# Performance work log

Hardware: AMD Instinct MI355X
Metric: run time of the kernel (lower is better)

The kernel has to match this reference:

```python
import jax, jax.numpy as jnp
import numpy as np

B, N, D, H = 32, 8192, 128, 128


def setup_inputs() -> dict:
    key = jax.random.key(0)
    ks = jax.random.split(key, 9)
    s = lambda k, shp, fan: jax.random.normal(k, shp, jnp.float32) / np.sqrt(fan)
    return {
        "x": jax.random.normal(ks[0], (B, N, D), jnp.float32),
        "Wg1": s(ks[1], (D, H), D), "bg1": jnp.zeros((H,), jnp.float32),
        "Wg2": s(ks[2], (H, 1), H), "bg2": jnp.zeros((1,), jnp.float32),
        "Wn1": s(ks[3], (D, H), D), "bn1": jnp.zeros((H,), jnp.float32),
        "Wn2": s(ks[4], (H, H), H), "bn2": jnp.zeros((H,), jnp.float32),
    }


def reference(x, Wg1, bg1, Wg2, bg2, Wn1, bn1, Wn2, bn2):
    # gate_nn: Linear -> SiLU -> Linear(->1); scores per node
    gate = jnp.einsum("bnd,dh->bnh", x, Wg1) + bg1
    gate = jax.nn.silu(gate)
    gate = jnp.einsum("bnh,ho->bno", gate, Wg2) + bg2  # [B,N,1]
    # nn: Linear -> SiLU -> Linear; transformed node features
    h = jax.nn.silu(jnp.einsum("bnd,dh->bnh", x, Wn1) + bn1)
    h = jnp.einsum("bnh,hk->bnk", h, Wn2) + bn2  # [B,N,H]
    # segment softmax over nodes of each graph (segments == batch dim here)
    attn = jax.nn.softmax(gate, axis=1)  # [B,N,1]
    # weighted-sum pooling per graph
    return jnp.sum(attn * h, axis=1)  # [B,H]
```

## Files before the change

### kernel.cpp

```cpp
#include <hip/hip_runtime.h>

#define B_ 32
#define N_ 8192
#define D_ 128
#define H_ 128
#define R_ (B_ * N_)

#define NBLK 4096

typedef _Float16 f16;
typedef __attribute__((ext_vector_type(4))) _Float16 f16x4;
typedef __attribute__((ext_vector_type(8))) _Float16 f16x8;
typedef __attribute__((ext_vector_type(4))) float f32x4;

static constexpr size_t WPACK_OFF = 0;
static constexpr size_t VPART_OFF = 98304;
static constexpr size_t SPART_OFF = VPART_OFF + (size_t)NBLK * 128 * 4;

__device__ __forceinline__ float silu_f(float v) {
    return v * __builtin_amdgcn_rcpf(1.0f + __expf(-v));
}

__device__ __forceinline__ f32x4 mfma16(f16x8 a, f16x8 b, f32x4 c) {
    return __builtin_amdgcn_mfma_f32_16x16x32_f16(a, b, c, 0, 0, 0);
}

__global__ void k0_prepack(const float* __restrict__ Wg1,
                           const float* __restrict__ Wn1,
                           const float* __restrict__ Wn2,
                           f16* __restrict__ wp) {
    int tid = blockIdx.x * 256 + threadIdx.x;
    int m    = tid >> 14;
    int r    = tid & 16383;
    int j    = r & 7;
    int lane = (r >> 3) & 63;
    int kc   = (r >> 9) & 3;
    int nt   = r >> 11;
    int k = kc * 32 + (lane >> 4) * 8 + j;
    int n = nt * 16 + (lane & 15);
    const float* W = (m == 0) ? Wg1 : (m == 1) ? Wn1 : Wn2;
    wp[tid] = (f16)W[k * 128 + n];
}

__global__ __launch_bounds__(256, 3) void k1_fused(
        const float* __restrict__ x,
        const float* __restrict__ bg1, const float* __restrict__ wg2,
        const float* __restrict__ bg2, const float* __restrict__ bn1,
        const f16* __restrict__ wp,
        float* __restrict__ vpart, float* __restrict__ spart) {
    __shared__ f16 xlds[64 * 128];
    __shared__ f16 h1lds[64 * 128];
    __shared__ float gpart[4][64];

    const int tid  = threadIdx.x;
    const int w    = tid >> 6;
    const int lane = tid & 63;
    const int q    = lane >> 4;
    const int c    = lane & 15;

    const long rowbase = (long)blockIdx.x * 64;
    const float4* xg = (const float4*)x + rowbase * 32;
    float4 xv[8];
#pragma unroll
    for (int s = 0; s < 8; ++s) xv[s] = xg[s * 256 + tid];

    const f16x8* wpv = (const f16x8*)wp;
    f16x8 fg1[2][4], fn1[2][4];
#pragma unroll
    for (int s = 0; s < 2; ++s)
#pragma unroll
        for (int kc = 0; kc < 4; ++kc) {
            int base = ((2 * w + s) * 4 + kc) * 64 + lane;
            fg1[s][kc] = wpv[base];
            fn1[s][kc] = wpv[2048 + base];
        }
    float bg1q[2][4], wg2q[2][4], bn1q[2][4];
#pragma unroll
    for (int s = 0; s < 2; ++s)
#pragma unroll
        for (int r = 0; r < 4; ++r) {
            int col = (2 * w + s) * 16 + q * 4 + r;
            bg1q[s][r] = bg1[col];
            wg2q[s][r] = wg2[col];
            bn1q[s][r] = bn1[col];
        }
    const float bg2v = bg2[0];

    const int loh_e = (q * 16 + (c ^ q)) * 8;
    const int loh_o = (q * 16 + (c ^ (q | 4))) * 8;
    int h1wb[2];
#pragma unroll
    for (int s = 0; s < 2; ++s) {
        int q2 = s * 2 + (q >> 1);
        int v2 = ((w & 1) << 2) | q2;
        h1wb[s] = w * 512 + (q2 * 16 + (c ^ v2)) * 8 + (q & 1) * 4;
    }

#pragma unroll
    for (int s = 0; s < 8; ++s) {
        int e   = s * 256 + tid;
        int row = e >> 5, c4 = e & 31;
        int mt = row >> 4, cc = row & 15;
        int kc = c4 >> 3, qq = (c4 >> 1) & 3, j = (c4 & 1) * 4;
        int sw = (c4 >> 1) & 7;
        float4 vv = xv[s];
        f16x4 hv = {(f16)vv.x, (f16)vv.y, (f16)vv.z, (f16)vv.w};
        *(f16x4*)&xlds[((mt * 4 + kc) * 64 + qq * 16 + (cc ^ sw)) * 8 + j] = hv;
    }
    __syncthreads();

#pragma unroll
    for (int mt = 0; mt < 4; ++mt) {
        f16x8 a[4];
#pragma unroll
        for (int kc = 0; kc < 4; ++kc)
            a[kc] = *(const f16x8*)&xlds[(mt * 4 + kc) * 512 +
                                         ((kc & 1) ? loh_o : loh_e)];
        f32x4 ag[2] = {{0.f,0.f,0.f,0.f},{0.f,0.f,0.f,0.f}};
        f32x4 an[2] = {{0.f,0.f,0.f,0.f},{0.f,0.f,0.f,0.f}};
#pragma unroll
        for (int kc = 0; kc < 4; ++kc) {
#pragma unroll
            for (int s = 0; s < 2; ++s) {
                ag[s] = mfma16(fg1[s][kc], a[kc], ag[s]);
                an[s] = mfma16(fn1[s][kc], a[kc], an[s]);
            }
        }
#pragma unroll
        for (int s = 0; s < 2; ++s) {
            f16x4 h4;
#pragma unroll
            for (int r = 0; r < 4; ++r) h4[r] = (f16)silu_f(an[s][r] + bn1q[s][r]);
            *(f16x4*)&h1lds[mt * 2048 + h1wb[s]] = h4;
        }
        float p = 0.f;
#pragma unroll
        for (int s = 0; s < 2; ++s)
#pragma unroll
            for (int r = 0; r < 4; ++r)
                p += silu_f(ag[s][r] + bg1q[s][r]) * wg2q[s][r];
        p += __shfl_xor(p, 16);
        p += __shfl_xor(p, 32);
        if (lane < 16) gpart[w][mt * 16 + lane] = p;
    }

    f16x8 fn2[2][4];
#pragma unroll
    for (int s = 0; s < 2; ++s)
#pragma unroll
        for (int kc = 0; kc < 4; ++kc)
            fn2[s][kc] = wpv[4096 + ((2 * w + s) * 4 + kc) * 64 + lane];

    __syncthreads();

    float e4[4];
#pragma unroll
    for (int mt = 0; mt < 4; ++mt) {
        float g = bg2v + gpart[0][mt * 16 + c] + gpart[1][mt * 16 + c]
                       + gpart[2][mt * 16 + c] + gpart[3][mt * 16 + c];
        e4[mt] = __expf(g);
    }

    float V[2][4] = {{0.f,0.f,0.f,0.f},{0.f,0.f,0.f,0.f}};
#pragma unroll
    for (int mt = 0; mt < 4; ++mt) {
        f16x8 b[4];
#pragma unroll
        for (int kc = 0; kc < 4; ++kc)
            b[kc] = *(const f16x8*)&h1lds[(mt * 4 + kc) * 512 +
                                          ((kc & 1) ? loh_o : loh_e)];
        f32x4 acc[2] = {{0.f,0.f,0.f,0.f},{0.f,0.f,0.f,0.f}};
#pragma unroll
        for (int kc = 0; kc < 4; ++kc)
#pragma unroll
            for (int s = 0; s < 2; ++s)
                acc[s] = mfma16(fn2[s][kc], b[kc], acc[s]);
#pragma unroll
        for (int s = 0; s < 2; ++s)
#pragma unroll
            for (int r = 0; r < 4; ++r) V[s][r] += e4[mt] * acc[s][r];
    }

#pragma unroll
    for (int m = 1; m < 16; m <<= 1)
#pragma unroll
        for (int s = 0; s < 2; ++s)
#pragma unroll
            for (int r = 0; r < 4; ++r) V[s][r] += __shfl_xor(V[s][r], m);
    if (c == 0) {
#pragma unroll
        for (int s = 0; s < 2; ++s) {
            float4 o = {V[s][0], V[s][1], V[s][2], V[s][3]};
            *(float4*)&vpart[(long)blockIdx.x * 128 + (2 * w + s) * 16 + q * 4] = o;
        }
    }
    if (w == 0) {
        float Sl = e4[0] + e4[1] + e4[2] + e4[3];
#pragma unroll
        for (int m = 1; m < 16; m <<= 1) Sl += __shfl_xor(Sl, m);
        if (lane == 0) spart[blockIdx.x] = Sl;
    }
}

__global__ void k2_combine(const float* __restrict__ vpart,
                           const float* __restrict__ spart,
                           const float* __restrict__ bn2,
                           float* __restrict__ out) {
    const int b = blockIdx.x;
    const int t = threadIdx.x;
    const int j = t & 127;
    const int half = t >> 7;

    const float* vp = vpart + (long)b * 128 * 128;
    float v = 0.f;
#pragma unroll
    for (int k = 0; k < 64; ++k)
        v += vp[(half * 64 + k) * 128 + j];

    __shared__ float vred[128];
    __shared__ float sred[4];
    if (half == 0) vred[j] = v;

    float s = (t < 128) ? spart[b * 128 + t] : 0.f;
#pragma unroll
    for (int m = 1; m < 64; m <<= 1) s += __shfl_xor(s, m);
    if (t < 128 && (t & 63) == 0) sred[t >> 6] = s;
    __syncthreads();
    if (half == 1) vred[j] += v;
    __syncthreads();
    if (t < 128) {
        float denom = sred[0] + sred[1];
        out[b * 128 + t] = vred[t] / denom + bn2[t];
    }
}

extern "C" void kernel_launch(void* const* d_in, const int* in_sizes, int n_in,
                              void* d_out, int out_size, void* d_ws, size_t ws_size,
                              hipStream_t stream) {
    const float* x   = (const float*)d_in[0];
    const float* Wg1 = (const float*)d_in[1];
    const float* bg1 = (const float*)d_in[2];
    const float* Wg2 = (const float*)d_in[3];
    const float* bg2 = (const float*)d_in[4];
    const float* Wn1 = (const float*)d_in[5];
    const float* bn1 = (const float*)d_in[6];
    const float* Wn2 = (const float*)d_in[7];
    const float* bn2 = (const float*)d_in[8];
    float* out = (float*)d_out;

    char* ws = (char*)d_ws;
    f16*   wp    = (f16*)(ws + WPACK_OFF);
    float* vpart = (float*)(ws + VPART_OFF);
    float* spart = (float*)(ws + SPART_OFF);

    k0_prepack<<<192, 256, 0, stream>>>(Wg1, Wn1, Wn2, wp);
    k1_fused<<<NBLK, 256, 0, stream>>>(x, bg1, Wg2, bg2, bn1, wp, vpart, spart);
    k2_combine<<<32, 256, 0, stream>>>(vpart, spart, bn2, out);
}
```

Baseline: 212.0 us.

## Load x fragments directly from global into MFMA registers, dropping LDS staging

Removes the shared-memory staging buffer for x. Each wave now loads its own MFMA A-fragments straight from global memory and double-buffers the next row tile's loads in registers. This removes an LDS write/read round trip and a block barrier. In exchange, every wave redundantly reads the full 64x128 x tile (4x the global/L2 traffic), global loads become strided per lane, and register pressure rises, so launch bounds drop from 3 to 2 blocks per CU.

```diff
diff --git a/kernel.cpp b/kernel.cpp
--- a/kernel.cpp
+++ b/kernel.cpp
@@ -42,13 +42,12 @@
     wp[tid] = (f16)W[k * 128 + n];
 }
 
-__global__ __launch_bounds__(256, 3) void k1_fused(
+__global__ __launch_bounds__(256, 2) void k1_fused(
         const float* __restrict__ x,
         const float* __restrict__ bg1, const float* __restrict__ wg2,
         const float* __restrict__ bg2, const float* __restrict__ bn1,
         const f16* __restrict__ wp,
         float* __restrict__ vpart, float* __restrict__ spart) {
-    __shared__ f16 xlds[64 * 128];
     __shared__ f16 h1lds[64 * 128];
     __shared__ float gpart[4][64];
 
@@ -59,10 +58,8 @@
     const int c    = lane & 15;
 
     const long rowbase = (long)blockIdx.x * 64;
-    const float4* xg = (const float4*)x + rowbase * 32;
-    float4 xv[8];
-#pragma unroll
-    for (int s = 0; s < 8; ++s) xv[s] = xg[s * 256 + tid];
+    const float4* __restrict__ xr = (const float4*)x;
+    const long fragbase = (rowbase + c) * 32 + q * 2;
 
     const f16x8* wpv = (const f16x8*)wp;
     f16x8 fg1[2][4], fn1[2][4];
@@ -96,26 +93,32 @@
         h1wb[s] = w * 512 + (q2 * 16 + (c ^ v2)) * 8 + (q & 1) * 4;
     }
 
-#pragma unroll
-    for (int s = 0; s < 8; ++s) {
-        int e   = s * 256 + tid;
-        int row = e >> 5, c4 = e & 31;
-        int mt = row >> 4, cc = row & 15;
-        int kc = c4 >> 3, qq = (c4 >> 1) & 3, j = (c4 & 1) * 4;
-        int sw = (c4 >> 1) & 7;
-        float4 vv = xv[s];
-        f16x4 hv = {(f16)vv.x, (f16)vv.y, (f16)vv.z, (f16)vv.w};
-        *(f16x4*)&xlds[((mt * 4 + kc) * 64 + qq * 16 + (cc ^ sw)) * 8 + j] = hv;
-    }
-    __syncthreads();
+    float4 xb[2][8];
+#pragma unroll
+    for (int kc = 0; kc < 4; ++kc) {
+        xb[0][kc * 2]     = xr[fragbase + kc * 8];
+        xb[0][kc * 2 + 1] = xr[fragbase + kc * 8 + 1];
+    }
 
 #pragma unroll
     for (int mt = 0; mt < 4; ++mt) {
+        const int cur = mt & 1, nxt = cur ^ 1;
+        if (mt < 3) {
+            const long fb = fragbase + (long)(mt + 1) * 16 * 32;
+#pragma unroll
+            for (int kc = 0; kc < 4; ++kc) {
+                xb[nxt][kc * 2]     = xr[fb + kc * 8];
+                xb[nxt][kc * 2 + 1] = xr[fb + kc * 8 + 1];
+            }
+        }
         f16x8 a[4];
 #pragma unroll
-        for (int kc = 0; kc < 4; ++kc)
-            a[kc] = *(const f16x8*)&xlds[(mt * 4 + kc) * 512 +
-                                         ((kc & 1) ? loh_o : loh_e)];
+        for (int kc = 0; kc < 4; ++kc) {
+            float4 u = xb[cur][kc * 2], v = xb[cur][kc * 2 + 1];
+            f16x8 t = {(f16)u.x, (f16)u.y, (f16)u.z, (f16)u.w,
+                       (f16)v.x, (f16)v.y, (f16)v.z, (f16)v.w};
+            a[kc] = t;
+        }
         f32x4 ag[2] = {{0.f,0.f,0.f,0.f},{0.f,0.f,0.f,0.f}};
         f32x4 an[2] = {{0.f,0.f,0.f,0.f},{0.f,0.f,0.f,0.f}};
 #pragma unroll
```

Result: slower. 245.2 us (+15.7%).

## Split fused MLP-pool kernel into gate/first-layer and second-layer pooling kernels

Applied to the files above, without the earlier changes.

Splits the single fused kernel in two. The first computes the gate scores, their exponentials and the SiLU hidden layer, writing the hidden activations to global memory in fp16 in MFMA fragment order. A second kernel then runs the second linear layer and the weighted pooling over four tiles per block. The combine kernel is reworked for the new partial layout. The goal is lower LDS and register pressure and better occupancy per kernel, at the cost of an extra global round trip for the hidden activations and an extra launch.

```diff
diff --git a/kernel.cpp b/kernel.cpp
--- a/kernel.cpp
+++ b/kernel.cpp
@@ -6,7 +6,8 @@
 #define H_ 128
 #define R_ (B_ * N_)
 
-#define NBLK 4096
+#define NBLKA 4096
+#define NBLKB 1024
 
 typedef _Float16 f16;
 typedef __attribute__((ext_vector_type(4))) _Float16 f16x4;
@@ -14,8 +15,10 @@
 typedef __attribute__((ext_vector_type(4))) float f32x4;
 
 static constexpr size_t WPACK_OFF = 0;
-static constexpr size_t VPART_OFF = 98304;
-static constexpr size_t SPART_OFF = VPART_OFF + (size_t)NBLK * 128 * 4;
+static constexpr size_t EWS_OFF   = 98304;
+static constexpr size_t VPART_OFF = EWS_OFF + (size_t)R_ * 4;
+static constexpr size_t SPART_OFF = VPART_OFF + (size_t)NBLKB * 128 * 4;
+static constexpr size_t H1WS_OFF  = 2097152;
 
 __device__ __forceinline__ float silu_f(float v) {
     return v * __builtin_amdgcn_rcpf(1.0f + __expf(-v));
@@ -42,14 +45,14 @@
     wp[tid] = (f16)W[k * 128 + n];
 }
 
-__global__ __launch_bounds__(256, 3) void k1_fused(
+__global__ __launch_bounds__(256, 3) void k1_gate_n1(
         const float* __restrict__ x,
         const float* __restrict__ bg1, const float* __restrict__ wg2,
         const float* __restrict__ bg2, const float* __restrict__ bn1,
         const f16* __restrict__ wp,
-        float* __restrict__ vpart, float* __restrict__ spart) {
+        f16* __restrict__ h1ws, float* __restrict__ ews,
+        float* __restrict__ spart) {
     __shared__ f16 xlds[64 * 128];
-    __shared__ f16 h1lds[64 * 128];
     __shared__ float gpart[4][64];
 
     const int tid  = threadIdx.x;
@@ -88,13 +91,11 @@
 
     const int loh_e = (q * 16 + (c ^ q)) * 8;
     const int loh_o = (q * 16 + (c ^ (q | 4))) * 8;
-    int h1wb[2];
-#pragma unroll
-    for (int s = 0; s < 2; ++s) {
-        int q2 = s * 2 + (q >> 1);
-        int v2 = ((w & 1) << 2) | q2;
-        h1wb[s] = w * 512 + (q2 * 16 + (c ^ v2)) * 8 + (q & 1) * 4;
-    }
+    long h1b[2];
+#pragma unroll
+    for (int s = 0; s < 2; ++s)
+        h1b[s] = (long)blockIdx.x * 8192 +
+                 (w * 64 + (s * 2 + (q >> 1)) * 16 + c) * 8 + (q & 1) * 4;
 
 #pragma unroll
     for (int s = 0; s < 8; ++s) {
@@ -131,7 +132,7 @@
             f16x4 h4;
 #pragma unroll
             for (int r = 0; r < 4; ++r) h4[r] = (f16)silu_f(an[s][r] + bn1q[s][r]);
-            *(f16x4*)&h1lds[mt * 2048 + h1wb[s]] = h4;
+            *(f16x4*)&h1ws[h1b[s] + mt * 2048] = h4;
         }
         float p = 0.f;
 #pragma unroll
@@ -143,7 +144,30 @@
         p += __shfl_xor(p, 32);
         if (lane < 16) gpart[w][mt * 16 + lane] = p;
     }
-
+    __syncthreads();
+
+    if (tid < 64) {
+        float g = bg2v + gpart[0][tid] + gpart[1][tid]
+                       + gpart[2][tid] + gpart[3][tid];
+        float e = __expf(g);
+        ews[rowbase + tid] = e;
+        float Sl = e;
+#pragma unroll
+        for (int m = 1; m < 64; m <<= 1) Sl += __shfl_xor(Sl, m);
+        if (tid == 0) spart[blockIdx.x] = Sl;
+    }
+}
+
+__global__ __launch_bounds__(256, 4) void k3_n2pool(
+        const f16* __restrict__ h1ws, const float* __restrict__ ews,
+        const f16* __restrict__ wp, float* __restrict__ vpart) {
+    const int tid  = threadIdx.x;
+    const int w    = tid >> 6;
+    const int lane = tid & 63;
+    const int q    = lane >> 4;
+    const int c    = lane & 15;
+
+    const f16x8* wpv = (const f16x8*)wp;
     f16x8 fn2[2][4];
 #pragma unroll
     for (int s = 0; s < 2; ++s)
@@ -151,34 +175,31 @@
         for (int kc = 0; kc < 4; ++kc)
             fn2[s][kc] = wpv[4096 + ((2 * w + s) * 4 + kc) * 64 + lane];
 
-    __syncthreads();
-
-    float e4[4];
-#pragma unroll
-    for (int mt = 0; mt < 4; ++mt) {
-        float g = bg2v + gpart[0][mt * 16 + c] + gpart[1][mt * 16 + c]
-                       + gpart[2][mt * 16 + c] + gpart[3][mt * 16 + c];
-        e4[mt] = __expf(g);
-    }
-
+    const f16x8* __restrict__ hp = (const f16x8*)h1ws;
     float V[2][4] = {{0.f,0.f,0.f,0.f},{0.f,0.f,0.f,0.f}};
-#pragma unroll
-    for (int mt = 0; mt < 4; ++mt) {
-        f16x8 b[4];
-#pragma unroll
-        for (int kc = 0; kc < 4; ++kc)
-            b[kc] = *(const f16x8*)&h1lds[(mt * 4 + kc) * 512 +
-                                          ((kc & 1) ? loh_o : loh_e)];
-        f32x4 acc[2] = {{0.f,0.f,0.f,0.f},{0.f,0.f,0.f,0.f}};
-#pragma unroll
-        for (int kc = 0; kc < 4; ++kc)
+
+    const int t0 = blockIdx.x * 4;
+#pragma unroll
+    for (int ti = 0; ti < 4; ++ti) {
+        const long tile = t0 + ti;
+#pragma unroll
+        for (int mt = 0; mt < 4; ++mt) {
+            const long fb = (tile * 16 + mt * 4) * 64 + lane;
+            f16x8 b[4];
+#pragma unroll
+            for (int kc = 0; kc < 4; ++kc) b[kc] = hp[fb + kc * 64];
+            float e = ews[tile * 64 + mt * 16 + c];
+            f32x4 acc[2] = {{0.f,0.f,0.f,0.f},{0.f,0.f,0.f,0.f}};
+#pragma unroll
+            for (int kc = 0; kc < 4; ++kc)
+#pragma unroll
+                for (int s = 0; s < 2; ++s)
+                    acc[s] = mfma16(fn2[s][kc], b[kc], acc[s]);
 #pragma unroll
             for (int s = 0; s < 2; ++s)
-                acc[s] = mfma16(fn2[s][kc], b[kc], acc[s]);
-#pragma unroll
-        for (int s = 0; s < 2; ++s)
-#pragma unroll
-            for (int r = 0; r < 4; ++r) V[s][r] += e4[mt] * acc[s][r];
+#pragma unroll
+                for (int r = 0; r < 4; ++r) V[s][r] += e * acc[s][r];
+        }
     }
 
 #pragma unroll
@@ -193,12 +214,6 @@
             float4 o = {V[s][0], V[s][1], V[s][2], V[s][3]};
             *(float4*)&vpart[(long)blockIdx.x * 128 + (2 * w + s) * 16 + q * 4] = o;
         }
-    }
-    if (w == 0) {
-        float Sl = e4[0] + e4[1] + e4[2] + e4[3];
-#pragma unroll
-        for (int m = 1; m < 16; m <<= 1) Sl += __shfl_xor(Sl, m);
-        if (lane == 0) spart[blockIdx.x] = Sl;
     }
 }
 
@@ -208,30 +223,20 @@
                            float* __restrict__ out) {
     const int b = blockIdx.x;
     const int t = threadIdx.x;
-    const int j = t & 127;
-    const int half = t >> 7;
-
-    const float* vp = vpart + (long)b * 128 * 128;
+
     float v = 0.f;
 #pragma unroll
-    for (int k = 0; k < 64; ++k)
-        v += vp[(half * 64 + k) * 128 + j];
-
-    __shared__ float vred[128];
-    __shared__ float sred[4];
-    if (half == 0) vred[j] = v;
-
-    float s = (t < 128) ? spart[b * 128 + t] : 0.f;
+    for (int k = 0; k < 32; ++k)
+        v += vpart[(long)(b * 32 + k) * 128 + t];
+
+    float s = spart[b * 128 + t];
 #pragma unroll
     for (int m = 1; m < 64; m <<= 1) s += __shfl_xor(s, m);
-    if (t < 128 && (t & 63) == 0) sred[t >> 6] = s;
+    __shared__ float sred[2];
+    if ((t & 63) == 0) sred[t >> 6] = s;
     __syncthreads();
-    if (half == 1) vred[j] += v;
-    __syncthreads();
-    if (t < 128) {
-        float denom = sred[0] + sred[1];
-        out[b * 128 + t] = vred[t] / denom + bn2[t];
-    }
+    float denom = sred[0] + sred[1];
+    out[b * 128 + t] = v / denom + bn2[t];
 }
 
 extern "C" void kernel_launch(void* const* d_in, const int* in_sizes, int n_in,
@@ -250,10 +255,14 @@
 
     char* ws = (char*)d_ws;
     f16*   wp    = (f16*)(ws + WPACK_OFF);
+    float* ews   = (float*)(ws + EWS_OFF);
     float* vpart = (float*)(ws + VPART_OFF);
     float* spart = (float*)(ws + SPART_OFF);
+    f16*   h1ws  = (f16*)(ws + H1WS_OFF);
 
     k0_prepack<<<192, 256, 0, stream>>>(Wg1, Wn1, Wn2, wp);
-    k1_fused<<<NBLK, 256, 0, stream>>>(x, bg1, Wg2, bg2, bn1, wp, vpart, spart);
-    k2_combine<<<32, 256, 0, stream>>>(vpart, spart, bn2, out);
-}
+    k1_gate_n1<<<NBLKA, 256, 0, stream>>>(x, bg1, Wg2, bg2, bn1, wp,
+                                          h1ws, ews, spart);
+    k3_n2pool<<<NBLKB, 256, 0, stream>>>(h1ws, ews, wp, vpart);
+    k2_combine<<<32, 128, 0, stream>>>(vpart, spart, bn2, out);
+}
```

Result: slower. 235.8 us (+11.2%).
